# Optimization experiments

Measured on AMD Instinct MI355X. Metric: run time of the kernel, lower is better.

The kernel has to match this reference:

```python
import jax, jax.numpy as jnp
import numpy as np
from jax import lax

B, C_IN, C_OUT, H, W = 32, 96, 96, 56, 56
E = 8          # num_experts
HID = 576      # round(96 * 6)
K = 3          # depthwise kernel size


def setup_inputs() -> dict:
    key = jax.random.key(0)
    ks = jax.random.split(key, 12)
    f = lambda k, s, sc=0.05: jax.random.normal(k, s, dtype=jnp.float32) * sc
    return {
        "x": jax.random.normal(ks[0], (B, C_IN, H, W), dtype=jnp.float32),
        # router for expand conv (input = x, C_IN channels)
        "w_r1": f(ks[1], (E, C_IN)), "b_r1": jnp.zeros((E,), jnp.float32),
        # expert bank for 1x1 expand: [E, HID, C_IN]
        "w1": f(ks[2], (E, HID, C_IN)),
        "g1": jnp.ones((HID,), jnp.float32), "bt1": jnp.zeros((HID,), jnp.float32),
        "m1": f(ks[3], (HID,), 0.01), "v1": jax.random.uniform(ks[4], (HID,), dtype=jnp.float32) + 0.5,
        # router for depthwise conv (input = expanded features, HID channels)
        "w_r2": f(ks[5], (E, HID)), "b_r2": jnp.zeros((E,), jnp.float32),
        # expert bank for depthwise 3x3: [E, HID, K, K] (in/groups = 1)
        "w2": f(ks[6], (E, HID, K, K)),
        "g2": jnp.ones((HID,), jnp.float32), "bt2": jnp.zeros((HID,), jnp.float32),
        "m2": f(ks[7], (HID,), 0.01), "v2": jax.random.uniform(ks[8], (HID,), dtype=jnp.float32) + 0.5,
        # expert bank for 1x1 project: [E, C_OUT, HID]
        "w3": f(ks[9], (E, C_OUT, HID)),
        "g3": jnp.ones((C_OUT,), jnp.float32), "bt3": jnp.zeros((C_OUT,), jnp.float32),
        "m3": f(ks[10], (C_OUT,), 0.01), "v3": jax.random.uniform(ks[11], (C_OUT,), dtype=jnp.float32) + 0.5,
        # block-level router (input = x, C_IN channels) gating the project conv
        "w_r3": f(jax.random.fold_in(key, 99), (E, C_IN)), "b_r3": jnp.zeros((E,), jnp.float32),
    }


def _route(feat, Wf, bf):
    # BasicRouter: global avg pool -> Linear -> sigmoid. feat: [B, C, H, W] -> [B, E]
    return jax.nn.sigmoid(feat.mean(axis=(2, 3)) @ Wf.T + bf)


def _bn(y, g, b, m, v, eps=1e-5):
    inv = g * lax.rsqrt(v + eps)
    return y * inv[None, :, None, None] + (b - m * inv)[None, :, None, None]


def reference(x, w_r1, b_r1, w1, g1, bt1, m1, v1,
              w_r2, b_r2, w2, g2, bt2, m2, v2,
              w3, g3, bt3, m3, v3, w_r3, b_r3):
    r1 = _route(x, w_r1, b_r1)      # [B, E] gate for expand conv
    r_blk = _route(x, w_r3, b_r3)   # [B, E] block router gates project conv

    # --- CondConv 1x1 expand: per-sample mixed kernel as batched GEMM ---
    w1c = jnp.einsum('be,eoc->boc', r1, w1)              # [B, HID, C_IN]
    y = jnp.einsum('bchw,boc->bohw', x, w1c)             # [B, HID, H, W]
    y = jnp.clip(_bn(y, g1, bt1, m1, v1), 0.0, 6.0)      # ReLU6

    # --- CondConv depthwise 3x3 (groups = HID), router on expanded feats ---
    r2 = _route(y, w_r2, b_r2)                           # [B, E]
    kw = jnp.einsum('be,eckl->bckl', r2, w2).reshape(B * HID, 1, K, K)
    y = lax.conv_general_dilated(
        y.reshape(1, B * HID, H, W), kw, (1, 1), 'SAME',
        dimension_numbers=('NCHW', 'OIHW', 'NCHW'),
        feature_group_count=B * HID).reshape(B, HID, H, W)
    y = jnp.clip(_bn(y, g2, bt2, m2, v2), 0.0, 6.0)

    # --- CondConv 1x1 project, gated by the block router(x) ---
    w3c = jnp.einsum('be,eoc->boc', r_blk, w3)           # [B, C_OUT, HID]
    y = jnp.einsum('bchw,boc->bohw', y, w3c)             # [B, C_OUT, H, W]
    y = _bn(y, g3, bt3, m3, v3)

    return x + y  # stride==1 and inp==oup -> residual connection
```

## Files before the change

kernel.cpp:

```cpp
#include <hip/hip_runtime.h>
#include <hip/hip_bf16.h>

#define B_   32
#define CIN  96
#define COUT 96
#define NP   3136
#define NE   8
#define HIDD 576

typedef short bf16x8 __attribute__((ext_vector_type(8)));
typedef float f32x4 __attribute__((ext_vector_type(4)));

__device__ __forceinline__ unsigned short f2bf(float f) {
  __hip_bfloat16 h = __float2bfloat16(f);
  unsigned short u; __builtin_memcpy(&u, &h, 2); return u;
}
__device__ __forceinline__ float u2f(unsigned int v) {
  float f; __builtin_memcpy(&f, &v, 4); return f;
}

__global__ __launch_bounds__(256) void k_transpose(const float* __restrict__ x,
                                                   unsigned short* __restrict__ xt,
                                                   float* __restrict__ xpart) {
  __shared__ float tile[CIN][65];
  int bi = blockIdx.x; int b = bi / 49, pt = bi % 49; int p0 = pt * 64;
  int t = threadIdx.x;
  for (int j = t; j < CIN * 64; j += 256) {
    int c = j >> 6, pi = j & 63;
    tile[c][pi] = x[((size_t)(b * CIN + c)) * NP + p0 + pi];
  }
  __syncthreads();
  if (t < CIN) {
    float s = 0.f;
    for (int i = 0; i < 64; ++i) s += tile[t][i];
    xpart[((size_t)(b * 49 + pt)) * CIN + t] = s;
  }
  for (int j = t; j < 64 * CIN; j += 256) {
    int p = j / CIN, c = j % CIN;
    xt[((size_t)(b * NP + p0 + p)) * CIN + c] = f2bf(tile[c][p]);
  }
}

__global__ __launch_bounds__(64) void k_front(const float* __restrict__ xpart,
    const float* __restrict__ wr1, const float* __restrict__ br1,
    const float* __restrict__ wr3, const float* __restrict__ br3,
    float* __restrict__ r1, float* __restrict__ rblk,
    const float* g1, const float* bt1, const float* m1, const float* v1,
    const float* g2, const float* bt2, const float* m2, const float* v2,
    const float* g3, const float* bt3, const float* m3, const float* v3,
    float* sc1, float* bi1, float* sc2, float* bi2, float* sc3, float* bi3) {
  int bi = blockIdx.x; int lane = threadIdx.x;
  if (bi < 512) {
    const float* wr; const float* br; float* dst; int id;
    if (bi < 256) { wr = wr1; br = br1; dst = r1;   id = bi; }
    else          { wr = wr3; br = br3; dst = rblk; id = bi - 256; }
    int b = id >> 3, e = id & 7;
    float s = 0.f;
    for (int c = lane; c < CIN; c += 64) {
      const float* xp = xpart + (size_t)b * 49 * CIN + c;
      float xm = 0.f;
#pragma unroll 7
      for (int k = 0; k < 49; ++k) xm += xp[k * CIN];
      s += xm * (1.0f / NP) * wr[e * CIN + c];
    }
    s += __shfl_xor(s, 1);  s += __shfl_xor(s, 2);  s += __shfl_xor(s, 4);
    s += __shfl_xor(s, 8);  s += __shfl_xor(s, 16); s += __shfl_xor(s, 32);
    if (lane == 0) dst[id] = 1.0f / (1.0f + __expf(-(s + br[e])));
  } else {
    int i = (bi - 512) * 64 + lane;
    if (i < HIDD) {
      float s = g1[i] * rsqrtf(v1[i] + 1e-5f); sc1[i] = s; bi1[i] = bt1[i] - m1[i] * s;
    } else if (i < 2 * HIDD) {
      int c = i - HIDD;
      float s = g2[c] * rsqrtf(v2[c] + 1e-5f); sc2[c] = s; bi2[c] = bt2[c] - m2[c] * s;
    } else if (i < 2 * HIDD + COUT) {
      int c = i - 2 * HIDD;
      float s = g3[c] * rsqrtf(v3[c] + 1e-5f); sc3[c] = s; bi3[c] = bt3[c] - m3[c] * s;
    }
  }
}

__global__ __launch_bounds__(256) void k_mixw(
    const float* __restrict__ w1, const float* __restrict__ r1, unsigned short* __restrict__ w1c,
    const float* __restrict__ w3, const float* __restrict__ rblk, unsigned short* __restrict__ w3c) {
  __shared__ float rsh[256];
  int bi = blockIdx.x; int t = threadIdx.x;
  const float* w; const float* r; unsigned short* dst; int oc0;
  if (bi < 216) { w = w1; r = r1;   dst = w1c; oc0 = bi * 256; }
  else          { w = w3; r = rblk; dst = w3c; oc0 = (bi - 216) * 256; }
  rsh[t] = r[t];
  __syncthreads();
  int oc = oc0 + t;
  float wv[NE];
#pragma unroll
  for (int e = 0; e < NE; ++e) wv[e] = w[(size_t)e * 55296 + oc];
  for (int b = 0; b < B_; ++b) {
    float a = 0.f;
#pragma unroll
    for (int e = 0; e < NE; ++e) a += rsh[b * 8 + e] * wv[e];
    dst[(size_t)b * 55296 + oc] = f2bf(a);
  }
}

__global__ __launch_bounds__(256) void k_expand2(const unsigned short* __restrict__ xt,
    const unsigned short* __restrict__ w1c, const float* __restrict__ sc1,
    const float* __restrict__ bi1, unsigned short* __restrict__ y2,
    float* __restrict__ yspart) {
  __shared__ unsigned short As[64 * 104];
  __shared__ unsigned short Bs[64 * 104];
  int t = threadIdx.x;
  int pt = blockIdx.x;
  int p0 = pt * 64, o0 = blockIdx.y * 64, b = blockIdx.z;
  const unsigned short* ag = w1c + (size_t)b * 55296 + (size_t)o0 * 96;
  const unsigned short* bg = xt + ((size_t)b * NP + p0) * 96;
  for (int j = t; j < 768; j += 256) {
    int r = j / 12, ch = j % 12;
    *(int4*)(As + r * 104 + ch * 8) = *(const int4*)(ag + r * 96 + ch * 8);
    *(int4*)(Bs + r * 104 + ch * 8) = *(const int4*)(bg + r * 96 + ch * 8);
  }
  __syncthreads();
  int lane = t & 63, wv = t >> 6;
  int m = lane & 15, q = lane >> 4;
  f32x4 acc[4];
#pragma unroll
  for (int nt = 0; nt < 4; ++nt) acc[nt] = 0.f;
#pragma unroll
  for (int kk = 0; kk < 3; ++kk) {
    bf16x8 af = *(const bf16x8*)(As + (wv * 16 + m) * 104 + kk * 32 + q * 8);
#pragma unroll
    for (int nt = 0; nt < 4; ++nt) {
      bf16x8 bfb = *(const bf16x8*)(Bs + (nt * 16 + m) * 104 + kk * 32 + q * 8);
      acc[nt] = __builtin_amdgcn_mfma_f32_16x16x32_bf16(af, bfb, acc[nt], 0, 0, 0);
    }
  }
  __syncthreads();
  float sc[4], bb[4];
#pragma unroll
  for (int i = 0; i < 4; ++i) {
    int o = o0 + wv * 16 + q * 4 + i;
    sc[i] = sc1[o]; bb[i] = bi1[o];
  }
  float rs[4] = {0.f, 0.f, 0.f, 0.f};
  unsigned short* T = As;
#pragma unroll
  for (int nt = 0; nt < 4; ++nt) {
    unsigned short pk[4];
#pragma unroll
    for (int i = 0; i < 4; ++i) {
      float v = acc[nt][i] * sc[i] + bb[i];
      v = fminf(fmaxf(v, 0.f), 6.f);
      rs[i] += v;
      pk[i] = f2bf(v);
    }
    uint2 pv; __builtin_memcpy(&pv, pk, 8);
    *(uint2*)(T + (nt * 16 + m) * 72 + wv * 16 + q * 4) = pv;
  }
#pragma unroll
  for (int i = 0; i < 4; ++i) {
    float r = rs[i];
    r += __shfl_xor(r, 1); r += __shfl_xor(r, 2);
    r += __shfl_xor(r, 4); r += __shfl_xor(r, 8);
    if (m == 0)
      yspart[((size_t)b * 49 + pt) * HIDD + o0 + wv * 16 + q * 4 + i] = r;
  }
  __syncthreads();
  for (int j = t; j < 512; j += 256) {
    int r = j >> 3, ch = j & 7;
    *(int4*)(y2 + ((size_t)(b * NP + p0 + r)) * 576 + o0 + ch * 8) =
        *(const int4*)(T + r * 72 + ch * 8);
  }
}

__global__ __launch_bounds__(256) void k_mid(const float* __restrict__ yspart,
    const float* __restrict__ wr2, const float* __restrict__ br2,
    const float* __restrict__ w2, const float* __restrict__ sc2,
    const float* __restrict__ bi2, float* __restrict__ kwt) {
  __shared__ float ysum_l[HIDD];
  __shared__ float r2_l[NE];
  int b = blockIdx.x, t = threadIdx.x;
  const float* yp = yspart + (size_t)b * 49 * HIDD;
  for (int c = t; c < HIDD; c += 256) {
    float s = 0.f;
#pragma unroll 7
    for (int k = 0; k < 49; ++k) s += yp[k * HIDD + c];
    ysum_l[c] = s;
  }
  __syncthreads();
  int wv = t >> 6, lane = t & 63;
  for (int e = wv; e < NE; e += 4) {
    float s = 0.f;
    for (int h = lane; h < HIDD; h += 64)
      s += ysum_l[h] * (1.0f / NP) * wr2[e * HIDD + h];
    s += __shfl_xor(s, 1);  s += __shfl_xor(s, 2);  s += __shfl_xor(s, 4);
    s += __shfl_xor(s, 8);  s += __shfl_xor(s, 16); s += __shfl_xor(s, 32);
    if (lane == 0) r2_l[e] = 1.0f / (1.0f + __expf(-(s + br2[e])));
  }
  __syncthreads();
  float rr[NE];
#pragma unroll
  for (int e = 0; e < NE; ++e) rr[e] = r2_l[e];
  for (int c = t; c < HIDD; c += 256) {
    float sc = sc2[c];
    float* dst = kwt + (size_t)b * 5760 + c;
#pragma unroll
    for (int k = 0; k < 9; ++k) {
      float s = 0.f;
#pragma unroll
      for (int e = 0; e < NE; ++e) s += rr[e] * w2[((size_t)e * HIDD + c) * 9 + k];
      dst[k * 576] = s * sc;
    }
    dst[9 * 576] = bi2[c];
  }
}

__device__ __forceinline__ f32x4 cvt4(uint2 v) {
  f32x4 r;
  r[0] = u2f(v.x << 16); r[1] = u2f(v.x & 0xffff0000u);
  r[2] = u2f(v.y << 16); r[3] = u2f(v.y & 0xffff0000u);
  return r;
}
__device__ __forceinline__ uint2 pack4(f32x4 v) {
  uint2 r;
  r.x = (unsigned)f2bf(v[0]) | ((unsigned)f2bf(v[1]) << 16);
  r.y = (unsigned)f2bf(v[2]) | ((unsigned)f2bf(v[3]) << 16);
  return r;
}
__device__ __forceinline__ f32x4 clamp6(f32x4 v) {
#pragma unroll
  for (int i = 0; i < 4; ++i) v[i] = fminf(fmaxf(v[i], 0.f), 6.f);
  return v;
}

__global__ __launch_bounds__(512, 4) void k_dwproj(const unsigned short* __restrict__ y2,
    const float* __restrict__ kwt, const unsigned short* __restrict__ w3c,
    const float* __restrict__ sc3, const float* __restrict__ bi3,
    const float* __restrict__ x, float* __restrict__ out) {
  __shared__ unsigned short zl[56 * 584];
  __shared__ unsigned short As[96 * 72];
  int t = threadIdx.x;
  int h = blockIdx.x, b = blockIdx.z;
  const unsigned short* ag = w3c + (size_t)b * 55296;

  int r0 = t >> 3, c8 = t & 7;
  int r1 = 64 + (t >> 3);
  bool two = (t < 256);
  int4 ra0, ra1;
#define LOADA(kc) do {                                                       \
    ra0 = *(const int4*)(ag + (size_t)r0 * 576 + (kc) * 64 + c8 * 8);        \
    if (two) ra1 = *(const int4*)(ag + (size_t)r1 * 576 + (kc) * 64 + c8 * 8); \
  } while (0)
#define WRITEA() do {                                                        \
    *(int4*)(As + r0 * 72 + c8 * 8) = ra0;                                   \
    if (two) *(int4*)(As + r1 * 72 + c8 * 8) = ra1;                          \
  } while (0)

  LOADA(0);

  {
    bool okU = (h > 0), okD = (h < 55);
    int rU = okU ? (h - 1) : h;
    int rD = okD ? (h + 1) : h;
    f32x4 d0, d1, d2;
#pragma unroll 1
    for (int task = t; task < 576; task += 512) {
      int cgi = task % 144;
      int seg = task / 144;
      int c = cgi * 4, w0 = seg * 14;
      const float* kp = kwt + (size_t)b * 5760 + c;
      f32x4 tk[9], tb;
#pragma unroll
      for (int k = 0; k < 9; ++k) tk[k] = *(const f32x4*)(kp + k * 576);
      tb = *(const f32x4*)(kp + 9 * 576);
      const unsigned short* yrU = y2 + ((size_t)(b * NP + rU * 56)) * 576 + c;
      const unsigned short* yrC = y2 + ((size_t)(b * NP + h  * 56)) * 576 + c;
      const unsigned short* yrD = y2 + ((size_t)(b * NP + rD * 56)) * 576 + c;

#define LOADC3(j) do {                                                       \
      uint2 q0, q1, q2;                                                      \
      q0.x = q0.y = q1.x = q1.y = q2.x = q2.y = 0u;                          \
      if ((unsigned)(j) < 56u) {                                             \
        if (okU) q0 = *(const uint2*)(yrU + (size_t)(j) * 576);              \
        q1 = *(const uint2*)(yrC + (size_t)(j) * 576);                       \
        if (okD) q2 = *(const uint2*)(yrD + (size_t)(j) * 576);              \
      }                                                                      \
      d0 = cvt4(q0); d1 = cvt4(q1); d2 = cvt4(q2);                           \
    } while (0)

#define SCAT3(A, Bv, Cv, j, STORE) do {                                      \
      LOADC3(j);                                                             \
      A  += d0 * tk[2] + d1 * tk[5] + d2 * tk[8];                            \
      Bv += d0 * tk[1] + d1 * tk[4] + d2 * tk[7];                            \
      Cv += d0 * tk[0] + d1 * tk[3] + d2 * tk[6];                            \
      if (STORE)                                                             \
        *(uint2*)(zl + (size_t)((j) - 1) * 584 + c) = pack4(clamp6(A));      \
      A = tb;                                                                \
    } while (0)

      f32x4 Av = tb, Bv = tb, Cv = tb;
      SCAT3(Av, Bv, Cv, w0 - 1, false);
      SCAT3(Bv, Cv, Av, w0,     false);
#pragma unroll 1
      for (int u = 0; u < 4; ++u) {
        int j = w0 + 1 + u * 3;
        SCAT3(Cv, Av, Bv, j,     true);
        SCAT3(Av, Bv, Cv, j + 1, true);
        SCAT3(Bv, Cv, Av, j + 2, true);
      }
      SCAT3(Cv, Av, Bv, w0 + 13, true);
      LOADC3(w0 + 14);
      Av += d0 * tk[2] + d1 * tk[5] + d2 * tk[8];
      *(uint2*)(zl + (size_t)(w0 + 13) * 584 + c) = pack4(clamp6(Av));
#undef SCAT3
#undef LOADC3
    }
  }

  WRITEA();
  __syncthreads();

  int lane = t & 63, wv = t >> 6;
  int wr = wv >> 2, wc = wv & 3;
  int m = lane & 15, q = lane >> 4;
  int px = wc * 16 + m;
  int pxr = (px < 56) ? px : 55;
  f32x4 acc0, acc1, acc2;
  acc0 = 0.f; acc1 = 0.f; acc2 = 0.f;

#define COMPUTE(kc) do {                                                     \
    _Pragma("unroll") for (int kk = 0; kk < 2; ++kk) {                       \
      bf16x8 bfv = *(const bf16x8*)(zl + (size_t)pxr * 584 + (kc) * 64 + kk * 32 + q * 8); \
      bf16x8 af0 = *(const bf16x8*)(As + (wr * 48 +  0 + m) * 72 + kk * 32 + q * 8); \
      bf16x8 af1 = *(const bf16x8*)(As + (wr * 48 + 16 + m) * 72 + kk * 32 + q * 8); \
      bf16x8 af2 = *(const bf16x8*)(As + (wr * 48 + 32 + m) * 72 + kk * 32 + q * 8); \
      acc0 = __builtin_amdgcn_mfma_f32_16x16x32_bf16(af0, bfv, acc0, 0, 0, 0); \
      acc1 = __builtin_amdgcn_mfma_f32_16x16x32_bf16(af1, bfv, acc1, 0, 0, 0); \
      acc2 = __builtin_amdgcn_mfma_f32_16x16x32_bf16(af2, bfv, acc2, 0, 0, 0); \
    } } while (0)

#pragma unroll 1
  for (int kc = 0; kc < 8; ++kc) {
    LOADA(kc + 1);
    COMPUTE(kc);
    __syncthreads();
    WRITEA();
    __syncthreads();
  }
  COMPUTE(8);

#undef COMPUTE
#undef LOADA
#undef WRITEA

  if (px < 56) {
    size_t pbase = (size_t)b * COUT * NP + (size_t)h * 56 + px;
#define EPI(ACC, a) do {                                                     \
    _Pragma("unroll") for (int i = 0; i < 4; ++i) {                          \
      int o = wr * 48 + (a) * 16 + q * 4 + i;                                \
      size_t idx = pbase + (size_t)o * NP;                                   \
      out[idx] = ACC[i] * sc3[o] + bi3[o] + x[idx];                          \
    } } while (0)
    EPI(acc0, 0); EPI(acc1, 1); EPI(acc2, 2);
#undef EPI
  }
}

#define OFF_XT     ((size_t)0)
#define OFF_KWT    OFF_XT
#define OFF_Y      ((size_t)19267584)
#define OFF_Z      ((size_t)134873088)
#define OFF_XPART  OFF_Z
#define OFF_YSPART (OFF_Z + 602112)
#define OFF_W1C    ((size_t)250478592)
#define OFF_W3C    ((size_t)254017536)
#define OFF_R1     ((size_t)257642496)
#define OFF_RBLK   ((size_t)257643520)
#define OFF_SC1    ((size_t)257645568)
#define OFF_BI1    ((size_t)257647872)
#define OFF_SC2    ((size_t)257650176)
#define OFF_BI2    ((size_t)257652480)
#define OFF_SC3    ((size_t)257654784)
#define OFF_BI3    ((size_t)257655168)

extern "C" void kernel_launch(void* const* d_in, const int* in_sizes, int n_in,
                              void* d_out, int out_size, void* d_ws, size_t ws_size,
                              hipStream_t stream) {
  const float* x   = (const float*)d_in[0];
  const float* wr1 = (const float*)d_in[1];
  const float* br1 = (const float*)d_in[2];
  const float* w1  = (const float*)d_in[3];
  const float* g1  = (const float*)d_in[4];
  const float* bt1 = (const float*)d_in[5];
  const float* m1  = (const float*)d_in[6];
  const float* v1  = (const float*)d_in[7];
  const float* wr2 = (const float*)d_in[8];
  const float* br2 = (const float*)d_in[9];
  const float* w2  = (const float*)d_in[10];
  const float* g2  = (const float*)d_in[11];
  const float* bt2 = (const float*)d_in[12];
  const float* m2  = (const float*)d_in[13];
  const float* v2  = (const float*)d_in[14];
  const float* w3  = (const float*)d_in[15];
  const float* g3  = (const float*)d_in[16];
  const float* bt3 = (const float*)d_in[17];
  const float* m3  = (const float*)d_in[18];
  const float* v3  = (const float*)d_in[19];
  const float* wr3 = (const float*)d_in[20];
  const float* br3 = (const float*)d_in[21];
  float* out = (float*)d_out;
  char* ws = (char*)d_ws;

  unsigned short* xt     = (unsigned short*)(ws + OFF_XT);
  unsigned short* y2     = (unsigned short*)(ws + OFF_Y);
  unsigned short* w1c    = (unsigned short*)(ws + OFF_W1C);
  unsigned short* w3c    = (unsigned short*)(ws + OFF_W3C);
  float* xpart  = (float*)(ws + OFF_XPART);
  float* yspart = (float*)(ws + OFF_YSPART);
  float* r1     = (float*)(ws + OFF_R1);
  float* rblk   = (float*)(ws + OFF_RBLK);
  float* sc1    = (float*)(ws + OFF_SC1);
  float* bi1    = (float*)(ws + OFF_BI1);
  float* sc2    = (float*)(ws + OFF_SC2);
  float* bi2    = (float*)(ws + OFF_BI2);
  float* sc3    = (float*)(ws + OFF_SC3);
  float* bi3    = (float*)(ws + OFF_BI3);
  float* kwt    = (float*)(ws + OFF_KWT);

  k_transpose<<<32 * 49, 256, 0, stream>>>(x, xt, xpart);
  k_front<<<532, 64, 0, stream>>>(xpart, wr1, br1, wr3, br3, r1, rblk,
                                  g1, bt1, m1, v1, g2, bt2, m2, v2, g3, bt3, m3, v3,
                                  sc1, bi1, sc2, bi2, sc3, bi3);
  k_mixw<<<432, 256, 0, stream>>>(w1, r1, w1c, w3, rblk, w3c);
  k_expand2<<<dim3(49, 9, 32), 256, 0, stream>>>(xt, w1c, sc1, bi1, y2, yspart);
  k_mid<<<32, 256, 0, stream>>>(yspart, wr2, br2, w2, sc2, bi2, kwt);
  k_dwproj<<<dim3(56, 1, 32), 512, 0, stream>>>(y2, kwt, w3c, sc3, bi3, x, out);
}
```

Before: 300.9 us.

## Load project weights directly into registers and use 576 threads for depthwise

The fused depthwise+project kernel now launches 576 threads so each thread handles exactly one depthwise task instead of looping with a tail. The project GEMM's A operand (mixed w3 weights) is read straight from global memory into registers with double buffering, removing the As LDS tile and the two __syncthreads per K-chunk. Row indices are also permuted across blocks. This removes barrier and LDS traffic but leaves one wave idle in the GEMM phase and relies on the cache to serve repeated weight reads.

```diff
diff --git a/kernel.cpp b/kernel.cpp
--- a/kernel.cpp
+++ b/kernel.cpp
@@ -231,136 +231,132 @@
   return v;
 }
 
-__global__ __launch_bounds__(512, 4) void k_dwproj(const unsigned short* __restrict__ y2,
+__global__ __launch_bounds__(576, 4) void k_dwproj(const unsigned short* __restrict__ y2,
     const float* __restrict__ kwt, const unsigned short* __restrict__ w3c,
     const float* __restrict__ sc3, const float* __restrict__ bi3,
     const float* __restrict__ x, float* __restrict__ out) {
   __shared__ unsigned short zl[56 * 584];
-  __shared__ unsigned short As[96 * 72];
   int t = threadIdx.x;
-  int h = blockIdx.x, b = blockIdx.z;
+  int hr = blockIdx.x, b = blockIdx.z;
+  int h = (hr & 7) * 7 + (hr >> 3);
   const unsigned short* ag = w3c + (size_t)b * 55296;
-
-  int r0 = t >> 3, c8 = t & 7;
-  int r1 = 64 + (t >> 3);
-  bool two = (t < 256);
-  int4 ra0, ra1;
-#define LOADA(kc) do {                                                       \
-    ra0 = *(const int4*)(ag + (size_t)r0 * 576 + (kc) * 64 + c8 * 8);        \
-    if (two) ra1 = *(const int4*)(ag + (size_t)r1 * 576 + (kc) * 64 + c8 * 8); \
-  } while (0)
-#define WRITEA() do {                                                        \
-    *(int4*)(As + r0 * 72 + c8 * 8) = ra0;                                   \
-    if (two) *(int4*)(As + r1 * 72 + c8 * 8) = ra1;                          \
-  } while (0)
-
-  LOADA(0);
 
   {
     bool okU = (h > 0), okD = (h < 55);
     int rU = okU ? (h - 1) : h;
     int rD = okD ? (h + 1) : h;
     f32x4 d0, d1, d2;
+    int task = t;
+    int cgi = task % 144;
+    int seg = task / 144;
+    int c = cgi * 4, w0 = seg * 14;
+    const float* kp = kwt + (size_t)b * 5760 + c;
+    f32x4 tk[9], tb;
+#pragma unroll
+    for (int k = 0; k < 9; ++k) tk[k] = *(const f32x4*)(kp + k * 576);
+    tb = *(const f32x4*)(kp + 9 * 576);
+    const unsigned short* yrU = y2 + ((size_t)(b * NP + rU * 56)) * 576 + c;
+    const unsigned short* yrC = y2 + ((size_t)(b * NP + h  * 56)) * 576 + c;
+    const unsigned short* yrD = y2 + ((size_t)(b * NP + rD * 56)) * 576 + c;
+
+#define LOADC3(j) do {                                                       \
+    uint2 q0, q1, q2;                                                        \
+    q0.x = q0.y = q1.x = q1.y = q2.x = q2.y = 0u;                            \
+    if ((unsigned)(j) < 56u) {                                               \
+      if (okU) q0 = *(const uint2*)(yrU + (size_t)(j) * 576);                \
+      q1 = *(const uint2*)(yrC + (size_t)(j) * 576);                         \
+      if (okD) q2 = *(const uint2*)(yrD + (size_t)(j) * 576);                \
+    }                                                                        \
+    d0 = cvt4(q0); d1 = cvt4(q1); d2 = cvt4(q2);                             \
+  } while (0)
+
+#define SCAT3(A, Bv, Cv, j, STORE) do {                                      \
+    LOADC3(j);                                                               \
+    A  += d0 * tk[2] + d1 * tk[5] + d2 * tk[8];                              \
+    Bv += d0 * tk[1] + d1 * tk[4] + d2 * tk[7];                              \
+    Cv += d0 * tk[0] + d1 * tk[3] + d2 * tk[6];                              \
+    if (STORE)                                                               \
+      *(uint2*)(zl + (size_t)((j) - 1) * 584 + c) = pack4(clamp6(A));        \
+    A = tb;                                                                  \
+  } while (0)
+
+    f32x4 Av = tb, Bv = tb, Cv = tb;
+    SCAT3(Av, Bv, Cv, w0 - 1, false);
+    SCAT3(Bv, Cv, Av, w0,     false);
 #pragma unroll 1
-    for (int task = t; task < 576; task += 512) {
-      int cgi = task % 144;
-      int seg = task / 144;
-      int c = cgi * 4, w0 = seg * 14;
-      const float* kp = kwt + (size_t)b * 5760 + c;
-      f32x4 tk[9], tb;
-#pragma unroll
-      for (int k = 0; k < 9; ++k) tk[k] = *(const f32x4*)(kp + k * 576);
-      tb = *(const f32x4*)(kp + 9 * 576);
-      const unsigned short* yrU = y2 + ((size_t)(b * NP + rU * 56)) * 576 + c;
-      const unsigned short* yrC = y2 + ((size_t)(b * NP + h  * 56)) * 576 + c;
-      const unsigned short* yrD = y2 + ((size_t)(b * NP + rD * 56)) * 576 + c;
-
-#define LOADC3(j) do {                                                       \
-      uint2 q0, q1, q2;                                                      \
-      q0.x = q0.y = q1.x = q1.y = q2.x = q2.y = 0u;                          \
-      if ((unsigned)(j) < 56u) {                                             \
-        if (okU) q0 = *(const uint2*)(yrU + (size_t)(j) * 576);              \
-        q1 = *(const uint2*)(yrC + (size_t)(j) * 576);                       \
-        if (okD) q2 = *(const uint2*)(yrD + (size_t)(j) * 576);              \
-      }                                                                      \
-      d0 = cvt4(q0); d1 = cvt4(q1); d2 = cvt4(q2);                           \
-    } while (0)
-
-#define SCAT3(A, Bv, Cv, j, STORE) do {                                      \
-      LOADC3(j);                                                             \
-      A  += d0 * tk[2] + d1 * tk[5] + d2 * tk[8];                            \
-      Bv += d0 * tk[1] + d1 * tk[4] + d2 * tk[7];                            \
-      Cv += d0 * tk[0] + d1 * tk[3] + d2 * tk[6];                            \
-      if (STORE)                                                             \
-        *(uint2*)(zl + (size_t)((j) - 1) * 584 + c) = pack4(clamp6(A));      \
-      A = tb;                                                                \
-    } while (0)
-
-      f32x4 Av = tb, Bv = tb, Cv = tb;
-      SCAT3(Av, Bv, Cv, w0 - 1, false);
-      SCAT3(Bv, Cv, Av, w0,     false);
-#pragma unroll 1
-      for (int u = 0; u < 4; ++u) {
-        int j = w0 + 1 + u * 3;
-        SCAT3(Cv, Av, Bv, j,     true);
-        SCAT3(Av, Bv, Cv, j + 1, true);
-        SCAT3(Bv, Cv, Av, j + 2, true);
-      }
-      SCAT3(Cv, Av, Bv, w0 + 13, true);
-      LOADC3(w0 + 14);
-      Av += d0 * tk[2] + d1 * tk[5] + d2 * tk[8];
-      *(uint2*)(zl + (size_t)(w0 + 13) * 584 + c) = pack4(clamp6(Av));
+    for (int u = 0; u < 4; ++u) {
+      int j = w0 + 1 + u * 3;
+      SCAT3(Cv, Av, Bv, j,     true);
+      SCAT3(Av, Bv, Cv, j + 1, true);
+      SCAT3(Bv, Cv, Av, j + 2, true);
+    }
+    SCAT3(Cv, Av, Bv, w0 + 13, true);
+    LOADC3(w0 + 14);
+    Av += d0 * tk[2] + d1 * tk[5] + d2 * tk[8];
+    *(uint2*)(zl + (size_t)(w0 + 13) * 584 + c) = pack4(clamp6(Av));
 #undef SCAT3
 #undef LOADC3
-    }
-  }
-
-  WRITEA();
+  }
+
   __syncthreads();
 
   int lane = t & 63, wv = t >> 6;
-  int wr = wv >> 2, wc = wv & 3;
-  int m = lane & 15, q = lane >> 4;
-  int px = wc * 16 + m;
-  int pxr = (px < 56) ? px : 55;
-  f32x4 acc0, acc1, acc2;
-  acc0 = 0.f; acc1 = 0.f; acc2 = 0.f;
-
-#define COMPUTE(kc) do {                                                     \
-    _Pragma("unroll") for (int kk = 0; kk < 2; ++kk) {                       \
-      bf16x8 bfv = *(const bf16x8*)(zl + (size_t)pxr * 584 + (kc) * 64 + kk * 32 + q * 8); \
-      bf16x8 af0 = *(const bf16x8*)(As + (wr * 48 +  0 + m) * 72 + kk * 32 + q * 8); \
-      bf16x8 af1 = *(const bf16x8*)(As + (wr * 48 + 16 + m) * 72 + kk * 32 + q * 8); \
-      bf16x8 af2 = *(const bf16x8*)(As + (wr * 48 + 32 + m) * 72 + kk * 32 + q * 8); \
-      acc0 = __builtin_amdgcn_mfma_f32_16x16x32_bf16(af0, bfv, acc0, 0, 0, 0); \
-      acc1 = __builtin_amdgcn_mfma_f32_16x16x32_bf16(af1, bfv, acc1, 0, 0, 0); \
-      acc2 = __builtin_amdgcn_mfma_f32_16x16x32_bf16(af2, bfv, acc2, 0, 0, 0); \
-    } } while (0)
-
+  if (wv < 8) {
+    int wr = wv >> 2, wc = wv & 3;
+    int m = lane & 15, q = lane >> 4;
+    int px = wc * 16 + m;
+    int pxr = (px < 56) ? px : 55;
+    const unsigned short* a0p = ag + (size_t)(wr * 48 +  0 + m) * 576 + q * 8;
+    const unsigned short* a1p = ag + (size_t)(wr * 48 + 16 + m) * 576 + q * 8;
+    const unsigned short* a2p = ag + (size_t)(wr * 48 + 32 + m) * 576 + q * 8;
+    f32x4 acc0, acc1, acc2;
+    acc0 = 0.f; acc1 = 0.f; acc2 = 0.f;
+    bf16x8 xa0, xa1, xa2, xa3, xa4, xa5;
+    bf16x8 ya0, ya1, ya2, ya3, ya4, ya5;
+
+#define LOADA(kc, A0, A1, A2, A3, A4, A5) do {                               \
+    A0 = *(const bf16x8*)(a0p + (kc) * 64);                                  \
+    A1 = *(const bf16x8*)(a0p + (kc) * 64 + 32);                             \
+    A2 = *(const bf16x8*)(a1p + (kc) * 64);                                  \
+    A3 = *(const bf16x8*)(a1p + (kc) * 64 + 32);                             \
+    A4 = *(const bf16x8*)(a2p + (kc) * 64);                                  \
+    A5 = *(const bf16x8*)(a2p + (kc) * 64 + 32);                             \
+  } while (0)
+
+#define COMPUTE(kc, A0, A1, A2, A3, A4, A5) do {                             \
+    bf16x8 b0 = *(const bf16x8*)(zl + (size_t)pxr * 584 + (kc) * 64 + q * 8);      \
+    bf16x8 b1 = *(const bf16x8*)(zl + (size_t)pxr * 584 + (kc) * 64 + 32 + q * 8); \
+    acc0 = __builtin_amdgcn_mfma_f32_16x16x32_bf16(A0, b0, acc0, 0, 0, 0);   \
+    acc1 = __builtin_amdgcn_mfma_f32_16x16x32_bf16(A2, b0, acc1, 0, 0, 0);   \
+    acc2 = __builtin_amdgcn_mfma_f32_16x16x32_bf16(A4, b0, acc2, 0, 0, 0);   \
+    acc0 = __builtin_amdgcn_mfma_f32_16x16x32_bf16(A1, b1, acc0, 0, 0, 0);   \
+    acc1 = __builtin_amdgcn_mfma_f32_16x16x32_bf16(A3, b1, acc1, 0, 0, 0);   \
+    acc2 = __builtin_amdgcn_mfma_f32_16x16x32_bf16(A5, b1, acc2, 0, 0, 0);   \
+  } while (0)
+
+    LOADA(0, xa0, xa1, xa2, xa3, xa4, xa5);
 #pragma unroll 1
-  for (int kc = 0; kc < 8; ++kc) {
-    LOADA(kc + 1);
-    COMPUTE(kc);
-    __syncthreads();
-    WRITEA();
-    __syncthreads();
-  }
-  COMPUTE(8);
-
+    for (int kc = 0; kc < 8; kc += 2) {
+      LOADA(kc + 1, ya0, ya1, ya2, ya3, ya4, ya5);
+      COMPUTE(kc, xa0, xa1, xa2, xa3, xa4, xa5);
+      LOADA(kc + 2, xa0, xa1, xa2, xa3, xa4, xa5);
+      COMPUTE(kc + 1, ya0, ya1, ya2, ya3, ya4, ya5);
+    }
+    COMPUTE(8, xa0, xa1, xa2, xa3, xa4, xa5);
 #undef COMPUTE
 #undef LOADA
-#undef WRITEA
-
-  if (px < 56) {
-    size_t pbase = (size_t)b * COUT * NP + (size_t)h * 56 + px;
+
+    if (px < 56) {
+      size_t pbase = (size_t)b * COUT * NP + (size_t)h * 56 + px;
 #define EPI(ACC, a) do {                                                     \
-    _Pragma("unroll") for (int i = 0; i < 4; ++i) {                          \
-      int o = wr * 48 + (a) * 16 + q * 4 + i;                                \
-      size_t idx = pbase + (size_t)o * NP;                                   \
-      out[idx] = ACC[i] * sc3[o] + bi3[o] + x[idx];                          \
-    } } while (0)
-    EPI(acc0, 0); EPI(acc1, 1); EPI(acc2, 2);
+      _Pragma("unroll") for (int i = 0; i < 4; ++i) {                        \
+        int o = wr * 48 + (a) * 16 + q * 4 + i;                              \
+        size_t idx = pbase + (size_t)o * NP;                                 \
+        out[idx] = ACC[i] * sc3[o] + bi3[o] + x[idx];                        \
+      } } while (0)
+      EPI(acc0, 0); EPI(acc1, 1); EPI(acc2, 2);
 #undef EPI
+    }
   }
 }
 
@@ -432,5 +428,5 @@
   k_mixw<<<432, 256, 0, stream>>>(w1, r1, w1c, w3, rblk, w3c);
   k_expand2<<<dim3(49, 9, 32), 256, 0, stream>>>(xt, w1c, sc1, bi1, y2, yspart);
   k_mid<<<32, 256, 0, stream>>>(yspart, wr2, br2, w2, sc2, bi2, kwt);
-  k_dwproj<<<dim3(56, 1, 32), 512, 0, stream>>>(y2, kwt, w3c, sc3, bi3, x, out);
-}
+  k_dwproj<<<dim3(56, 1, 32), 576, 0, stream>>>(y2, kwt, w3c, sc3, bi3, x, out);
+}
```

Result: slower. 350.8 us (+16.6%).
